# Optimization experiments

Measured on AMD Instinct MI355X. Metric: run time of the kernel, lower is better.

The kernel has to match this reference:

```python
import jax, jax.numpy as jnp
import numpy as np
from jax.ops import segment_sum, segment_max

N_NODES = 100000
N_EDGES = 1600000
F_DIM = 64
N_GRAPHS = 64
K_HOPS = 3
EPS = 1e-5


def setup_inputs() -> dict:
    key = jax.random.key(0)
    ks = jax.random.split(key, 8)
    x = jax.random.normal(ks[0], (N_NODES, F_DIM), dtype=jnp.float32)
    edge_index = jax.random.randint(ks[1], (2, N_EDGES), 0, N_NODES, dtype=jnp.int32)
    batch = jnp.sort(jax.random.randint(ks[2], (N_NODES,), 0, N_GRAPHS, dtype=jnp.int32))
    edge_weight = jax.random.uniform(ks[3], (N_EDGES,), dtype=jnp.float32)
    # TAGConv params: K+1 hop-wise linear weights (no per-lin bias) + one output bias
    W = jax.random.normal(ks[4], (K_HOPS + 1, F_DIM, F_DIM), dtype=jnp.float32) * 0.05
    b = jnp.zeros((F_DIM,), dtype=jnp.float32)
    # GraphNorm params
    gn_weight = jnp.ones((F_DIM,), dtype=jnp.float32)
    gn_bias = jnp.zeros((F_DIM,), dtype=jnp.float32)
    gn_mean_scale = jnp.ones((F_DIM,), dtype=jnp.float32)
    return {"x": x, "edge_index": edge_index, "batch": batch, "edge_weight": edge_weight,
            "W": W, "b": b, "gn_weight": gn_weight, "gn_bias": gn_bias,
            "gn_mean_scale": gn_mean_scale}


def reference(x, edge_index, batch, edge_weight, W, b, gn_weight, gn_bias, gn_mean_scale):
    src, dst = edge_index[0], edge_index[1]

    # --- TAGConv: gcn_norm without self-loops ---
    deg = segment_sum(edge_weight, dst, num_segments=N_NODES)            # [N]
    dis = jnp.where(deg > 0, jax.lax.rsqrt(deg), 0.0)                    # deg^{-1/2}, inf -> 0
    norm = dis[src] * edge_weight * dis[dst]                             # [E]

    # out = sum_k (A_norm^k x) W_k + b
    out = x @ W[0]
    h = x
    for k in range(1, K_HOPS + 1):
        h = segment_sum(norm[:, None] * h[src], dst, num_segments=N_NODES)  # [N, F]
        out = out + h @ W[k]
    out = out + b

    # --- GraphNorm: per-graph mean/var with learnable mean_scale ---
    cnt = segment_sum(jnp.ones((N_NODES,), out.dtype), batch, num_segments=N_GRAPHS)
    cnt = jnp.maximum(cnt, 1.0)[:, None]                                  # [G, 1]
    mean = segment_sum(out, batch, num_segments=N_GRAPHS) / cnt          # [G, F]
    centered = out - mean[batch] * gn_mean_scale                         # [N, F]
    var = segment_sum(centered * centered, batch, num_segments=N_GRAPHS) / cnt
    hn = gn_weight * centered / jnp.sqrt(var + EPS)[batch] + gn_bias

    # --- residual + ReLU (add_residue=True) ---
    h_emb = jax.nn.relu(hn + x)                                          # [N, F]

    # --- global mean + max pooling ---
    mean_pool = segment_sum(h_emb, batch, num_segments=N_GRAPHS) / cnt   # [G, F]
    max_pool = segment_max(h_emb, batch, num_segments=N_GRAPHS)          # [G, F]
    flat = jnp.concatenate([mean_pool, max_pool], axis=-1)               # [G, 2F]

    return (h_emb, flat)
```

## Files before the change

kernel.cpp:

```cpp
#include <hip/hip_runtime.h>
#include <hip/hip_bf16.h>

#define NN 100000
#define NE 1600000
#define NG 64
#define FD 64
#define EPSV 1e-5f

typedef __hip_bfloat16 bf16;
typedef __attribute__((ext_vector_type(8))) short bf16x8;
typedef __attribute__((ext_vector_type(4))) float f32x4;

__device__ __forceinline__ float ldb(bf16 v) { return __bfloat162float(v); }
__device__ __forceinline__ bf16 f2b(float v) { return __float2bfloat16(v); }
__device__ __forceinline__ float b2f_bits(short s) {
    return __uint_as_float(((unsigned)(unsigned short)s) << 16);
}

#define NB1 391
#define CB 625
#define EPB 2560
#define CCN (NB1 * CB)
#define SCB2 ((CCN + 2047) / 2048)

__device__ __forceinline__ int xcd_chunk(int bid, int nwg) {
    int q = nwg >> 3, r = nwg & 7;
    int xcd = bid & 7, j = bid >> 3;
    return (xcd < r ? xcd * (q + 1) : r * (q + 1) + (xcd - r) * q) + j;
}

constexpr size_t ALGN(size_t x) { return (x + 255) & ~(size_t)255; }
constexpr size_t OFF_GSUM = 0;
constexpr size_t OFF_GSSQ = OFF_GSUM + ALGN((size_t)NG * FD * 4);
constexpr size_t OFF_GCNT = OFF_GSSQ + ALGN((size_t)NG * FD * 4);
constexpr size_t OFF_PSUM = OFF_GCNT + ALGN((size_t)NG * 4);
constexpr size_t OFF_PMAX = OFF_PSUM + ALGN((size_t)NG * FD * 4);
constexpr size_t ZERO_BYTES = OFF_PMAX + ALGN((size_t)NG * FD * 4);
constexpr size_t OFF_CNT  = ZERO_BYTES;
constexpr size_t OFF_DIS  = OFF_CNT  + ALGN((size_t)NN * 4);
constexpr size_t OFF_ROWP = OFF_DIS  + ALGN((size_t)NN * 4);
constexpr size_t OFF_BSUM = OFF_ROWP + ALGN((size_t)NN * 4);
constexpr size_t OFF_WT   = OFF_BSUM + ALGN(256 * 4);
constexpr size_t OFF_CSR  = OFF_WT   + ALGN(16384 * 2);
constexpr size_t OFF_H    = OFF_CSR  + ALGN((size_t)NE * 8);
constexpr size_t OFF_OUT  = OFF_H    + ALGN((size_t)NN * 256 * 2);
constexpr size_t OFF_CSRT = OFF_OUT;
constexpr size_t OFF_CC   = OFF_CSRT + ALGN((size_t)NE * 8);
static_assert(OFF_CC + (size_t)CCN * 4 - OFF_OUT <= (size_t)NN * FD * 4, "alias overflow");

#define XCB 6250
__global__ __launch_bounds__(256) void coarse_fused_kernel(const int* __restrict__ dst,
                                                           int* __restrict__ cc,
                                                           const float* __restrict__ x,
                                                           bf16* __restrict__ H,
                                                           const float* __restrict__ W,
                                                           bf16* __restrict__ Wt) {
    int b = blockIdx.x;
    if (b < CB) {
        __shared__ int hist[NB1];
        for (int i = threadIdx.x; i < NB1; i += 256) hist[i] = 0;
        __syncthreads();
        int e0 = b * EPB + threadIdx.x;
        #pragma unroll
        for (int i = 0; i < EPB / 256; i++)
            atomicAdd(&hist[dst[e0 + i * 256] >> 8], 1);
        __syncthreads();
        for (int i = threadIdx.x; i < NB1; i += 256)
            cc[(size_t)i * CB + b] = hist[i];
    } else if (b < CB + XCB) {
        int i = (b - CB) * 256 + threadIdx.x;
        float4 xv = ((const float4*)x)[i];
        bf16 t0 = f2b(xv.x), t1 = f2b(xv.y), t2 = f2b(xv.z), t3 = f2b(xv.w);
        ushort4 o;
        o.x = *(unsigned short*)&t0; o.y = *(unsigned short*)&t1;
        o.z = *(unsigned short*)&t2; o.w = *(unsigned short*)&t3;
        ((ushort4*)H)[i] = o;
    } else {
        int i = (b - CB - XCB) * 256 + threadIdx.x;
        int n = i & 63, kk = i >> 6;
        Wt[n * 256 + kk] = f2b(W[kk * 64 + n]);
    }
}

#define SCAN_BLK 256
#define SCAN_ITEMS 8
__global__ __launch_bounds__(SCAN_BLK) void scan_blocks(int* __restrict__ data,
                                                        int* __restrict__ bsum, int n) {
    __shared__ int lds[SCAN_BLK];
    int t = threadIdx.x, b = blockIdx.x;
    int base = b * SCAN_BLK * SCAN_ITEMS + t * SCAN_ITEMS;
    int v[SCAN_ITEMS];
    int s = 0;
    #pragma unroll
    for (int i = 0; i < SCAN_ITEMS; i++) {
        int idx = base + i;
        v[i] = (idx < n) ? data[idx] : 0;
        s += v[i];
    }
    lds[t] = s;
    __syncthreads();
    for (int off = 1; off < SCAN_BLK; off <<= 1) {
        int x = (t >= off) ? lds[t - off] : 0;
        __syncthreads();
        lds[t] += x;
        __syncthreads();
    }
    int excl = lds[t] - s;
    if (t == SCAN_BLK - 1) bsum[b] = lds[t];
    int run = excl;
    #pragma unroll
    for (int i = 0; i < SCAN_ITEMS; i++) {
        int idx = base + i;
        if (idx < n) data[idx] = run;
        run += v[i];
    }
}

__global__ __launch_bounds__(256) void bsum_scan(int* __restrict__ bsum, int nb) {
    __shared__ int lds[256];
    int t = threadIdx.x;
    int v = (t < nb) ? bsum[t] : 0;
    lds[t] = v;
    __syncthreads();
    for (int off = 1; off < 256; off <<= 1) {
        int x = (t >= off) ? lds[t - off] : 0;
        __syncthreads();
        lds[t] += x;
        __syncthreads();
    }
    if (t < nb) bsum[t] = lds[t] - v;
}

__global__ __launch_bounds__(256) void scan_add2(int* __restrict__ data,
                                                 const int* __restrict__ bpref, int n) {
    int i = blockIdx.x * 256 + threadIdx.x;
    if (i >= n) return;
    data[i] += bpref[i >> 11];
}

__global__ __launch_bounds__(256) void scatter2_kernel(const int* __restrict__ src,
                                                       const int* __restrict__ dst,
                                                       const float* __restrict__ ew,
                                                       const int* __restrict__ cc,
                                                       int2* __restrict__ csrt) {
    __shared__ int sc[512];
    __shared__ int gdel[NB1];
    __shared__ int2 stage[EPB];
    __shared__ int sdel[EPB];
    int t = threadIdx.x;
    int L = xcd_chunk(blockIdx.x, CB);

    sc[t] = 0; sc[t + 256] = 0;
    __syncthreads();

    int br[EPB / 256], px[EPB / 256], pw[EPB / 256];
    #pragma unroll
    for (int i = 0; i < EPB / 256; i++) {
        int e = L * EPB + i * 256 + t;
        int d = dst[e];
        int bk = d >> 8;
        int rk = atomicAdd(&sc[bk], 1);
        br[i] = bk | (rk << 9);
        px[i] = src[e] | ((d & 255) << 17);
        pw[i] = __float_as_int(ew[e]);
    }
    __syncthreads();

    for (int off = 1; off < 512; off <<= 1) {
        int a0 = (t >= off) ? sc[t - off] : 0;
        int a1 = sc[t + 256 - off];
        __syncthreads();
        sc[t] += a0; sc[t + 256] += a1;
        __syncthreads();
    }

    for (int i = t; i < NB1; i += 256)
        gdel[i] = cc[(size_t)i * CB + L] - ((i > 0) ? sc[i - 1] : 0);
    __syncthreads();

    #pragma unroll
    for (int i = 0; i < EPB / 256; i++) {
        int bk = br[i] & 511;
        int rk = br[i] >> 9;
        int slot = ((bk > 0) ? sc[bk - 1] : 0) + rk;
        stage[slot] = make_int2(px[i], pw[i]);
        sdel[slot] = gdel[bk];
    }
    __syncthreads();

    for (int j = t; j < EPB; j += 256)
        csrt[(size_t)(sdel[j] + j)] = stage[j];
}

__global__ __launch_bounds__(256) void fine_kernel(const int* __restrict__ cc,
                                                   const int2* __restrict__ csrt,
                                                   int2* __restrict__ csr,
                                                   int* __restrict__ rowp,
                                                   int* __restrict__ cnts,
                                                   float* __restrict__ dis) {
    __shared__ int hist[256];
    __shared__ float degw[256];
    __shared__ int pref[256];
    __shared__ int fcur[256];
    int b = blockIdx.x;
    int t = threadIdx.x;
    int base = cc[(size_t)b * CB];
    int end = (b == NB1 - 1) ? NE : cc[(size_t)(b + 1) * CB];
    int cnt = end - base;
    hist[t] = 0; degw[t] = 0.f;
    __syncthreads();
    for (int j = t; j < cnt; j += 256) {
        int2 e = csrt[base + j];
        int f = e.x >> 17;
        atomicAdd(&hist[f], 1);
        atomicAdd(&degw[f], __int_as_float(e.y));
    }
    __syncthreads();
    int hv = hist[t];
    pref[t] = hv;
    __syncthreads();
    for (int off = 1; off < 256; off <<= 1) {
        int x = (t >= off) ? pref[t - off] : 0;
        __syncthreads();
        pref[t] += x;
        __syncthreads();
    }
    int ex = pref[t] - hv;
    fcur[t] = ex;
    int node = b * 256 + t;
    if (node < NN) {
        rowp[node] = base + ex;
        cnts[node] = hv;
        float s = degw[t];
        dis[node] = (s > 0.f) ? rsqrtf(s) : 0.f;
    }
    __syncthreads();
    for (int j = t; j < cnt; j += 256) {
        int2 e = csrt[base + j];
        int f = e.x >> 17;
        int pos = atomicAdd(&fcur[f], 1);
        csr[base + pos] = make_int2(e.x & 0x1FFFF, e.y);
    }
}

template <bool FIRST>
__device__ __forceinline__ void row_accum_gen(const bf16* __restrict__ hin,
                                              int2* cp, int cnt,
                                              const float* __restrict__ dis,
                                              int sub, int fl, float a[8]) {
    if (cnt <= 24) {
        int2 e0 = (sub < cnt) ? cp[sub] : make_int2(0, 0);
        int2 e1 = (8 + sub < cnt) ? cp[8 + sub] : make_int2(0, 0);
        int2 e2 = (16 + sub < cnt) ? cp[16 + sub] : make_int2(0, 0);
        bf16x8 v0 = *(const bf16x8*)(hin + (size_t)e0.x * 64 + fl * 8);
        bf16x8 v1 = *(const bf16x8*)(hin + (size_t)e1.x * 64 + fl * 8);
        bf16x8 v2 = *(const bf16x8*)(hin + (size_t)e2.x * 64 + fl * 8);
        float w0 = __int_as_float(e0.y);
        float w1 = __int_as_float(e1.y);
        float w2 = __int_as_float(e2.y);
        if (FIRST) {
            w0 *= dis[e0.x]; w1 *= dis[e1.x]; w2 *= dis[e2.x];
            if (fl == 0) {
                if (sub < cnt)      cp[sub].y      = __float_as_int(w0);
                if (8 + sub < cnt)  cp[8 + sub].y  = __float_as_int(w1);
                if (16 + sub < cnt) cp[16 + sub].y = __float_as_int(w2);
            }
        }
        #pragma unroll
        for (int i = 0; i < 8; i++)
            a[i] += w0 * b2f_bits(v0[i]) + w1 * b2f_bits(v1[i]) + w2 * b2f_bits(v2[i]);
    } else {
        float b[8] = {0, 0, 0, 0, 0, 0, 0, 0};
        int j = 0;
        for (; j + 16 <= cnt; j += 16) {
            int2 e0 = cp[j + sub];
            int2 e1 = cp[j + 8 + sub];
            bf16x8 v0 = *(const bf16x8*)(hin + (size_t)e0.x * 64 + fl * 8);
            bf16x8 v1 = *(const bf16x8*)(hin + (size_t)e1.x * 64 + fl * 8);
            float w0 = __int_as_float(e0.y);
            float w1 = __int_as_float(e1.y);
            if (FIRST) {
                w0 *= dis[e0.x]; w1 *= dis[e1.x];
                if (fl == 0) {
                    cp[j + sub].y     = __float_as_int(w0);
                    cp[j + 8 + sub].y = __float_as_int(w1);
                }
            }
            #pragma unroll
            for (int i = 0; i < 8; i++) a[i] += w0 * b2f_bits(v0[i]);
            #pragma unroll
            for (int i = 0; i < 8; i++) b[i] += w1 * b2f_bits(v1[i]);
        }
        for (; j < cnt; j += 8) {
            int jj = j + sub;
            int2 e = (jj < cnt) ? cp[jj] : make_int2(0, 0);
            bf16x8 v = *(const bf16x8*)(hin + (size_t)e.x * 64 + fl * 8);
            float w = __int_as_float(e.y);
            if (FIRST) {
                w *= dis[e.x];
                if (fl == 0 && jj < cnt) cp[jj].y = __float_as_int(w);
            }
            #pragma unroll
            for (int i = 0; i < 8; i++) a[i] += w * b2f_bits(v[i]);
        }
        #pragma unroll
        for (int i = 0; i < 8; i++) a[i] += b[i];
    }
}

template <bool FIRST>
__global__ __launch_bounds__(256) void hop_kernel(const bf16* __restrict__ hin,
                                                  bf16* __restrict__ hout,
                                                  const int* __restrict__ rowp,
                                                  const int* __restrict__ cnts,
                                                  int2* __restrict__ csr,
                                                  const float* __restrict__ dis) {
    int pair = blockIdx.x * 4 + (threadIdx.x >> 6);
    int rowA = pair * 2;
    if (rowA >= NN) return;
    rowA = __builtin_amdgcn_readfirstlane(rowA);
    int rowB = rowA + 1;
    int lane = threadIdx.x & 63;
    int sub = lane >> 3;
    int fl = lane & 7;

    int stA = rowp[rowA], cnA = cnts[rowA];
    int stB = rowp[rowB], cnB = cnts[rowB];
    float drA = dis[rowA], drB = dis[rowB];
    int2* cpA = csr + stA;
    int2* cpB = csr + stB;

    float a[8] = {0, 0, 0, 0, 0, 0, 0, 0};
    float c[8] = {0, 0, 0, 0, 0, 0, 0, 0};

    if (cnA <= 24 && cnB <= 24) {
        int2 eA0 = (sub < cnA) ? cpA[sub] : make_int2(0, 0);
        int2 eA1 = (8 + sub < cnA) ? cpA[8 + sub] : make_int2(0, 0);
        int2 eA2 = (16 + sub < cnA) ? cpA[16 + sub] : make_int2(0, 0);
        int2 eB0 = (sub < cnB) ? cpB[sub] : make_int2(0, 0);
        int2 eB1 = (8 + sub < cnB) ? cpB[8 + sub] : make_int2(0, 0);
        int2 eB2 = (16 + sub < cnB) ? cpB[16 + sub] : make_int2(0, 0);
        const bf16* hf = hin + fl * 8;
        bf16x8 vA0 = *(const bf16x8*)(hf + (size_t)eA0.x * 64);
        bf16x8 vA1 = *(const bf16x8*)(hf + (size_t)eA1.x * 64);
        bf16x8 vA2 = *(const bf16x8*)(hf + (size_t)eA2.x * 64);
        bf16x8 vB0 = *(const bf16x8*)(hf + (size_t)eB0.x * 64);
        bf16x8 vB1 = *(const bf16x8*)(hf + (size_t)eB1.x * 64);
        bf16x8 vB2 = *(const bf16x8*)(hf + (size_t)eB2.x * 64);
        float wA0 = __int_as_float(eA0.y);
        float wA1 = __int_as_float(eA1.y);
        float wA2 = __int_as_float(eA2.y);
        float wB0 = __int_as_float(eB0.y);
        float wB1 = __int_as_float(eB1.y);
        float wB2 = __int_as_float(eB2.y);
        if (FIRST) {
            wA0 *= dis[eA0.x]; wA1 *= dis[eA1.x]; wA2 *= dis[eA2.x];
            wB0 *= dis[eB0.x]; wB1 *= dis[eB1.x]; wB2 *= dis[eB2.x];
            if (fl == 0) {
                if (sub < cnA)      cpA[sub].y      = __float_as_int(wA0);
                if (8 + sub < cnA)  cpA[8 + sub].y  = __float_as_int(wA1);
                if (16 + sub < cnA) cpA[16 + sub].y = __float_as_int(wA2);
                if (sub < cnB)      cpB[sub].y      = __float_as_int(wB0);
                if (8 + sub < cnB)  cpB[8 + sub].y  = __float_as_int(wB1);
                if (16 + sub < cnB) cpB[16 + sub].y = __float_as_int(wB2);
            }
        }
        #pragma unroll
        for (int i = 0; i < 8; i++) {
            a[i] = wA0 * b2f_bits(vA0[i]) + wA1 * b2f_bits(vA1[i]) + wA2 * b2f_bits(vA2[i]);
            c[i] = wB0 * b2f_bits(vB0[i]) + wB1 * b2f_bits(vB1[i]) + wB2 * b2f_bits(vB2[i]);
        }
    } else {
        row_accum_gen<FIRST>(hin, cpA, cnA, dis, sub, fl, a);
        row_accum_gen<FIRST>(hin, cpB, cnB, dis, sub, fl, c);
    }

    #pragma unroll
    for (int i = 0; i < 8; i++) { a[i] += __shfl_xor(a[i], 8);  c[i] += __shfl_xor(c[i], 8); }
    #pragma unroll
    for (int i = 0; i < 8; i++) { a[i] += __shfl_xor(a[i], 16); c[i] += __shfl_xor(c[i], 16); }
    #pragma unroll
    for (int i = 0; i < 8; i++) { a[i] += __shfl_xor(a[i], 32); c[i] += __shfl_xor(c[i], 32); }

    if (sub == 0) {
        bf16x8 ovA, ovB;
        #pragma unroll
        for (int i = 0; i < 8; i++) {
            bf16 tA = f2b(a[i] * drA);
            bf16 tB = f2b(c[i] * drB);
            ovA[i] = *(short*)&tA;
            ovB[i] = *(short*)&tB;
        }
        *(bf16x8*)(hout + (size_t)rowA * 64 + fl * 8) = ovA;
        *(bf16x8*)(hout + (size_t)rowB * 64 + fl * 8) = ovB;
    }
}

#define GWAVES 1024
#define NT (NN / 16)

__global__ __launch_bounds__(256, 1) void gemm_kernel(const bf16* __restrict__ H,
                                                      const bf16* __restrict__ Wt,
                                                      const float* __restrict__ bias,
                                                      float* __restrict__ outb) {
    int wave = threadIdx.x >> 6;
    int lane = threadIdx.x & 63;
    int m = lane & 15, q = lane >> 4;
    int w = blockIdx.x * 4 + wave;

    bf16x8 B[4][8];
    #pragma unroll
    for (int n = 0; n < 4; n++) {
        const bf16* brow = Wt + (size_t)(n * 16 + m) * 256 + q * 8;
        #pragma unroll
        for (int ks = 0; ks < 8; ks++) B[n][ks] = *(const bf16x8*)(brow + ks * 32);
    }
    float bv[4];
    #pragma unroll
    for (int n = 0; n < 4; n++) bv[n] = bias[n * 16 + m];

    if (w >= NT) return;

    bf16x8 A0[8], A1[8];

    #define LOADA(dst_, t_)                                                      \
        {                                                                        \
            _Pragma("unroll")                                                    \
            for (int ks = 0; ks < 8; ks++)                                       \
                dst_[ks] = *(const bf16x8*)(H +                                  \
                    ((size_t)(ks >> 1) * NN + (size_t)((t_)*16 + m)) * 64 +      \
                    (ks & 1) * 32 + q * 8);                                      \
        }

    #define COMP(src_, t_)                                                   \
        {                                                                    \
            _Pragma("unroll")                                                \
            for (int n = 0; n < 4; n++) {                                    \
                f32x4 acc = {0.f, 0.f, 0.f, 0.f};                            \
                _Pragma("unroll")                                            \
                for (int ks = 0; ks < 8; ks++)                               \
                    acc = __builtin_amdgcn_mfma_f32_16x16x32_bf16(           \
                        src_[ks], B[n][ks], acc, 0, 0, 0);                   \
                _Pragma("unroll")                                            \
                for (int r = 0; r < 4; r++)                                  \
                    outb[(size_t)((t_)*16 + q * 4 + r) * 64 + n * 16 + m] =  \
                        acc[r] + bv[n];                                      \
            }                                                                \
        }

    int t = w;
    LOADA(A0, t)
    while (true) {
        int t1 = t + GWAVES;
        if (t1 < NT) LOADA(A1, t1)
        COMP(A0, t)
        if (t1 >= NT) return;
        int t2 = t1 + GWAVES;
        if (t2 < NT) LOADA(A0, t2)
        COMP(A1, t1)
        if (t2 >= NT) return;
        t = t2;
    }
    #undef LOADA
    #undef COMP
}

#define CH 32
#define STAT_WAVES ((NN + CH - 1) / CH)
#define STAT_BLOCKS ((STAT_WAVES * 64 + 255) / 256)

__global__ __launch_bounds__(256) void stats_kernel(const float* __restrict__ outb,
                                                    const int* __restrict__ batch,
                                                    float* __restrict__ gsum,
                                                    float* __restrict__ gssq,
                                                    float* __restrict__ gcnt) {
    int wid = (blockIdx.x * 256 + threadIdx.x) >> 6;
    int lane = threadIdx.x & 63;
    int n0 = wid * CH;
    if (n0 >= NN) return;
    int n1 = min(n0 + CH, NN);
    int g0 = batch[n0];
    if (n1 == n0 + CH && batch[n1 - 1] == g0) {
        float s = 0.f, s2 = 0.f;
        #pragma unroll
        for (int i = 0; i < CH; i++) {
            float v = outb[(size_t)(n0 + i) * 64 + lane];
            s += v; s2 += v * v;
        }
        atomicAdd(&gsum[g0 * 64 + lane], s);
        atomicAdd(&gssq[g0 * 64 + lane], s2);
        if (lane == 0) atomicAdd(&gcnt[g0], (float)CH);
    } else {
        int cur = g0; float s = 0.f, s2 = 0.f; int cl = 0;
        for (int i = n0; i < n1; i++) {
            int g = batch[i];
            if (g != cur) {
                atomicAdd(&gsum[cur * 64 + lane], s);
                atomicAdd(&gssq[cur * 64 + lane], s2);
                if (lane == 0) atomicAdd(&gcnt[cur], (float)cl);
                s = 0.f; s2 = 0.f; cl = 0; cur = g;
            }
            float v = outb[(size_t)i * 64 + lane];
            s += v; s2 += v * v; cl++;
        }
        atomicAdd(&gsum[cur * 64 + lane], s);
        atomicAdd(&gssq[cur * 64 + lane], s2);
        if (lane == 0) atomicAdd(&gcnt[cur], (float)cl);
    }
}

__device__ __forceinline__ void graph_mr(const float* gsum, const float* gssq,
                                         const float* gcnt, int g, int lane, float ms,
                                         float& mm, float& r) {
    float c = fmaxf(gcnt[g], 1.f);
    float mean = gsum[g * 64 + lane] / c;
    float msq = gssq[g * 64 + lane] / c;
    mm = mean * ms;
    float var = fmaxf(msq - 2.f * mm * mean + mm * mm, 0.f);
    r = rsqrtf(var + EPSV);
}

__global__ __launch_bounds__(256) void final_kernel(const float* __restrict__ outb,
                                                    const int* __restrict__ batch,
                                                    const float* __restrict__ xg,
                                                    const float* __restrict__ gsum,
                                                    const float* __restrict__ gssq,
                                                    const float* __restrict__ gcnt,
                                                    const float* __restrict__ gw_,
                                                    const float* __restrict__ gb_,
                                                    const float* __restrict__ ms_,
                                                    float* __restrict__ psum,
                                                    int* __restrict__ pmax,
                                                    float* __restrict__ hemb) {
    int wid = (blockIdx.x * 256 + threadIdx.x) >> 6;
    int lane = threadIdx.x & 63;
    int n0 = wid * CH;
    if (n0 >= NN) return;
    int n1 = min(n0 + CH, NN);
    float gw = gw_[lane], gb = gb_[lane], ms = ms_[lane];
    int g0 = batch[n0];
    if (n1 == n0 + CH && batch[n1 - 1] == g0) {
        float m, r;
        graph_mr(gsum, gssq, gcnt, g0, lane, ms, m, r);
        float ps = 0.f, pm = 0.f;
        #pragma unroll
        for (int i = 0; i < CH; i++) {
            size_t idx = (size_t)(n0 + i) * 64 + lane;
            float hn = gw * (outb[idx] - m) * r + gb;
            float he = hn + xg[idx];
            he = he > 0.f ? he : 0.f;
            hemb[idx] = he;
            ps += he;
            pm = fmaxf(pm, he);
        }
        atomicAdd(&psum[g0 * 64 + lane], ps);
        atomicMax(&pmax[g0 * 64 + lane], __float_as_int(pm));
    } else {
        int cur = g0;
        float m, r;
        graph_mr(gsum, gssq, gcnt, cur, lane, ms, m, r);
        float ps = 0.f, pm = 0.f;
        for (int i = n0; i < n1; i++) {
            int g = batch[i];
            if (g != cur) {
                atomicAdd(&psum[cur * 64 + lane], ps);
                atomicMax(&pmax[cur * 64 + lane], __float_as_int(pm));
                ps = 0.f; pm = 0.f; cur = g;
                graph_mr(gsum, gssq, gcnt, cur, lane, ms, m, r);
            }
            size_t idx = (size_t)i * 64 + lane;
            float hn = gw * (outb[idx] - m) * r + gb;
            float he = hn + xg[idx];
            he = he > 0.f ? he : 0.f;
            hemb[idx] = he;
            ps += he;
            pm = fmaxf(pm, he);
        }
        atomicAdd(&psum[cur * 64 + lane], ps);
        atomicMax(&pmax[cur * 64 + lane], __float_as_int(pm));
    }
}

__global__ __launch_bounds__(256) void pool_kernel(const float* __restrict__ psum,
                                                   const int* __restrict__ pmax,
                                                   const float* __restrict__ gcnt,
                                                   float* __restrict__ flat) {
    int i = blockIdx.x * 256 + threadIdx.x;
    if (i >= NG * FD) return;
    int g = i >> 6, f = i & 63;
    float c = fmaxf(gcnt[g], 1.f);
    flat[(size_t)g * 128 + f] = psum[i] / c;
    flat[(size_t)g * 128 + 64 + f] = __int_as_float(pmax[i]);
}

extern "C" void kernel_launch(void* const* d_in, const int* in_sizes, int n_in,
                              void* d_out, int out_size, void* d_ws, size_t ws_size,
                              hipStream_t stream) {
    const float* x = (const float*)d_in[0];
    const int* ei = (const int*)d_in[1];
    const int* batch = (const int*)d_in[2];
    const float* ew = (const float*)d_in[3];
    const float* W = (const float*)d_in[4];
    const float* bias = (const float*)d_in[5];
    const float* gnw = (const float*)d_in[6];
    const float* gnb = (const float*)d_in[7];
    const float* gms = (const float*)d_in[8];

    const int* src = ei;
    const int* dst = ei + NE;

    char* ws = (char*)d_ws;
    float* gsum = (float*)(ws + OFF_GSUM);
    float* gssq = (float*)(ws + OFF_GSSQ);
    float* gcnt = (float*)(ws + OFF_GCNT);
    float* psum = (float*)(ws + OFF_PSUM);
    int* pmax = (int*)(ws + OFF_PMAX);
    int* cnts = (int*)(ws + OFF_CNT);
    float* dis = (float*)(ws + OFF_DIS);
    int* rowp = (int*)(ws + OFF_ROWP);
    int* bsum = (int*)(ws + OFF_BSUM);
    bf16* Wt = (bf16*)(ws + OFF_WT);
    int2* csr = (int2*)(ws + OFF_CSR);
    bf16* H = (bf16*)(ws + OFF_H);
    float* outb = (float*)(ws + OFF_OUT);
    int2* csrt = (int2*)(ws + OFF_CSRT);
    int* cc = (int*)(ws + OFF_CC);

    float* hemb = (float*)d_out;
    float* flat = hemb + (size_t)NN * FD;

    hipMemsetAsync(d_ws, 0, ZERO_BYTES, stream);

    const size_t PL = (size_t)NN * 64;
    const int HOPB = (NN / 2 + 3) / 4;
    const int GFB = (NG * FD + 255) / 256;
    const int ADDB = (CCN + 255) / 256;

    coarse_fused_kernel<<<CB + XCB + 64, 256, 0, stream>>>(dst, cc, x, H, W, Wt);
    scan_blocks<<<SCB2, 256, 0, stream>>>(cc, bsum, CCN);
    bsum_scan<<<1, 256, 0, stream>>>(bsum, SCB2);
    scan_add2<<<ADDB, 256, 0, stream>>>(cc, bsum, CCN);
    scatter2_kernel<<<CB, 256, 0, stream>>>(src, dst, ew, cc, csrt);
    fine_kernel<<<NB1, 256, 0, stream>>>(cc, csrt, csr, rowp, cnts, dis);

    hop_kernel<true><<<HOPB, 256, 0, stream>>>(H, H + PL, rowp, cnts, csr, dis);
    hop_kernel<false><<<HOPB, 256, 0, stream>>>(H + PL, H + 2 * PL, rowp, cnts, csr, dis);
    hop_kernel<false><<<HOPB, 256, 0, stream>>>(H + 2 * PL, H + 3 * PL, rowp, cnts, csr, dis);

    gemm_kernel<<<GWAVES / 4, 256, 0, stream>>>(H, Wt, bias, outb);

    stats_kernel<<<STAT_BLOCKS, 256, 0, stream>>>(outb, batch, gsum, gssq, gcnt);
    final_kernel<<<STAT_BLOCKS, 256, 0, stream>>>(outb, batch, x, gsum, gssq, gcnt,
                                                  gnw, gnb, gms, psum, pmax, hemb);
    pool_kernel<<<GFB, 256, 0, stream>>>(psum, pmax, gcnt, flat);
}
```

Before: 329.3 us.

## Fold block-prefix scan into scatter/fine kernels and fuse graph stats into GEMM

Result: slower. 339.8 us (+3.2%).

```diff
diff --git a/kernel.cpp b/kernel.cpp
--- a/kernel.cpp
+++ b/kernel.cpp
@@ -116,34 +116,14 @@
     }
 }
 
-__global__ __launch_bounds__(256) void bsum_scan(int* __restrict__ bsum, int nb) {
-    __shared__ int lds[256];
-    int t = threadIdx.x;
-    int v = (t < nb) ? bsum[t] : 0;
-    lds[t] = v;
-    __syncthreads();
-    for (int off = 1; off < 256; off <<= 1) {
-        int x = (t >= off) ? lds[t - off] : 0;
-        __syncthreads();
-        lds[t] += x;
-        __syncthreads();
-    }
-    if (t < nb) bsum[t] = lds[t] - v;
-}
-
-__global__ __launch_bounds__(256) void scan_add2(int* __restrict__ data,
-                                                 const int* __restrict__ bpref, int n) {
-    int i = blockIdx.x * 256 + threadIdx.x;
-    if (i >= n) return;
-    data[i] += bpref[i >> 11];
-}
-
 __global__ __launch_bounds__(256) void scatter2_kernel(const int* __restrict__ src,
                                                        const int* __restrict__ dst,
                                                        const float* __restrict__ ew,
                                                        const int* __restrict__ cc,
+                                                       const int* __restrict__ bsum,
                                                        int2* __restrict__ csrt) {
     __shared__ int sc[512];
+    __shared__ int bp[128];
     __shared__ int gdel[NB1];
     __shared__ int2 stage[EPB];
     __shared__ int sdel[EPB];
@@ -151,6 +131,7 @@
     int L = xcd_chunk(blockIdx.x, CB);
 
     sc[t] = 0; sc[t + 256] = 0;
+    if (t < 128) bp[t] = (t < SCB2) ? bsum[t] : 0;
     __syncthreads();
 
     int br[EPB / 256], px[EPB / 256], pw[EPB / 256];
@@ -169,13 +150,19 @@
     for (int off = 1; off < 512; off <<= 1) {
         int a0 = (t >= off) ? sc[t - off] : 0;
         int a1 = sc[t + 256 - off];
+        int a2 = (off < 128 && t < 128 && t >= off) ? bp[t - off] : 0;
         __syncthreads();
         sc[t] += a0; sc[t + 256] += a1;
-        __syncthreads();
-    }
-
-    for (int i = t; i < NB1; i += 256)
-        gdel[i] = cc[(size_t)i * CB + L] - ((i > 0) ? sc[i - 1] : 0);
+        if (off < 128 && t < 128) bp[t] += a2;
+        __syncthreads();
+    }
+
+    for (int i = t; i < NB1; i += 256) {
+        int idx = i * CB + L;
+        int k = idx >> 11;
+        int gpref = (k > 0) ? bp[k - 1] : 0;
+        gdel[i] = cc[idx] + gpref - ((i > 0) ? sc[i - 1] : 0);
+    }
     __syncthreads();
 
     #pragma unroll
@@ -193,6 +180,7 @@
 }
 
 __global__ __launch_bounds__(256) void fine_kernel(const int* __restrict__ cc,
+                                                   const int* __restrict__ bsum,
                                                    const int2* __restrict__ csrt,
                                                    int2* __restrict__ csr,
                                                    int* __restrict__ rowp,
@@ -202,13 +190,32 @@
     __shared__ float degw[256];
     __shared__ int pref[256];
     __shared__ int fcur[256];
+    __shared__ int bp[128];
+    __shared__ int bounds[2];
     int b = blockIdx.x;
     int t = threadIdx.x;
-    int base = cc[(size_t)b * CB];
-    int end = (b == NB1 - 1) ? NE : cc[(size_t)(b + 1) * CB];
-    int cnt = end - base;
     hist[t] = 0; degw[t] = 0.f;
-    __syncthreads();
+    if (t < 128) bp[t] = (t < SCB2) ? bsum[t] : 0;
+    __syncthreads();
+    for (int off = 1; off < 128; off <<= 1) {
+        int x = (t < 128 && t >= off) ? bp[t - off] : 0;
+        __syncthreads();
+        if (t < 128) bp[t] += x;
+        __syncthreads();
+    }
+    if (t == 0) {
+        int i0 = b * CB, k0 = i0 >> 11;
+        bounds[0] = cc[i0] + ((k0 > 0) ? bp[k0 - 1] : 0);
+        if (b == NB1 - 1) bounds[1] = NE;
+        else {
+            int i1 = (b + 1) * CB, k1 = i1 >> 11;
+            bounds[1] = cc[i1] + ((k1 > 0) ? bp[k1 - 1] : 0);
+        }
+    }
+    __syncthreads();
+    int base = bounds[0];
+    int cnt = bounds[1] - base;
+
     for (int j = t; j < cnt; j += 256) {
         int2 e = csrt[base + j];
         int f = e.x >> 17;
@@ -402,6 +409,10 @@
 __global__ __launch_bounds__(256, 1) void gemm_kernel(const bf16* __restrict__ H,
                                                       const bf16* __restrict__ Wt,
                                                       const float* __restrict__ bias,
+                                                      const int* __restrict__ batch,
+                                                      float* __restrict__ gsum,
+                                                      float* __restrict__ gssq,
+                                                      float* __restrict__ gcnt,
                                                       float* __restrict__ outb) {
     int wave = threadIdx.x >> 6;
     int lane = threadIdx.x & 63;
@@ -432,20 +443,56 @@
                     (ks & 1) * 32 + q * 8);                                      \
         }
 
-    #define COMP(src_, t_)                                                   \
-        {                                                                    \
-            _Pragma("unroll")                                                \
-            for (int n = 0; n < 4; n++) {                                    \
-                f32x4 acc = {0.f, 0.f, 0.f, 0.f};                            \
-                _Pragma("unroll")                                            \
-                for (int ks = 0; ks < 8; ks++)                               \
-                    acc = __builtin_amdgcn_mfma_f32_16x16x32_bf16(           \
-                        src_[ks], B[n][ks], acc, 0, 0, 0);                   \
-                _Pragma("unroll")                                            \
-                for (int r = 0; r < 4; r++)                                  \
-                    outb[(size_t)((t_)*16 + q * 4 + r) * 64 + n * 16 + m] =  \
-                        acc[r] + bv[n];                                      \
-            }                                                                \
+    #define COMP(src_, t_)                                                          \
+        {                                                                           \
+            float s_[4], s2_[4], vals_[4][4];                                       \
+            _Pragma("unroll")                                                       \
+            for (int n = 0; n < 4; n++) {                                           \
+                f32x4 acc = {0.f, 0.f, 0.f, 0.f};                                   \
+                _Pragma("unroll")                                                   \
+                for (int ks = 0; ks < 8; ks++)                                      \
+                    acc = __builtin_amdgcn_mfma_f32_16x16x32_bf16(                  \
+                        src_[ks], B[n][ks], acc, 0, 0, 0);                          \
+                float ss = 0.f, ss2 = 0.f;                                          \
+                _Pragma("unroll")                                                   \
+                for (int r = 0; r < 4; r++) {                                       \
+                    float val = acc[r] + bv[n];                                     \
+                    vals_[n][r] = val;                                              \
+                    outb[(size_t)((t_)*16 + q * 4 + r) * 64 + n * 16 + m] = val;    \
+                    ss += val; ss2 += val * val;                                    \
+                }                                                                   \
+                s_[n] = ss; s2_[n] = ss2;                                           \
+            }                                                                       \
+            int gLo = batch[(t_)*16];                                               \
+            int gHi = batch[(t_)*16 + 15];                                          \
+            if (gLo == gHi) {                                                       \
+                _Pragma("unroll")                                                   \
+                for (int n = 0; n < 4; n++) {                                       \
+                    s_[n] += __shfl_xor(s_[n], 16);  s_[n] += __shfl_xor(s_[n], 32);   \
+                    s2_[n] += __shfl_xor(s2_[n], 16); s2_[n] += __shfl_xor(s2_[n], 32);\
+                }                                                                   \
+                if (q == 0) {                                                       \
+                    _Pragma("unroll")                                               \
+                    for (int n = 0; n < 4; n++) {                                   \
+                        atomicAdd(&gsum[gLo * 64 + n * 16 + m], s_[n]);             \
+                        atomicAdd(&gssq[gLo * 64 + n * 16 + m], s2_[n]);            \
+                    }                                                               \
+                }                                                                   \
+                if (lane == 0) atomicAdd(&gcnt[gLo], 16.f);                         \
+            } else {                                                               \
+                int4 b4 = *(const int4*)(batch + (t_)*16 + q * 4);                  \
+                int gr_[4] = {b4.x, b4.y, b4.z, b4.w};                              \
+                _Pragma("unroll")                                                   \
+                for (int r = 0; r < 4; r++) {                                       \
+                    _Pragma("unroll")                                               \
+                    for (int n = 0; n < 4; n++) {                                   \
+                        atomicAdd(&gsum[gr_[r] * 64 + n * 16 + m], vals_[n][r]);    \
+                        atomicAdd(&gssq[gr_[r] * 64 + n * 16 + m],                  \
+                                  vals_[n][r] * vals_[n][r]);                       \
+                    }                                                               \
+                }                                                                   \
+                if (lane < 16) atomicAdd(&gcnt[batch[(t_)*16 + lane]], 1.f);        \
+            }                                                                       \
         }
 
     int t = w;
@@ -468,46 +515,6 @@
 #define CH 32
 #define STAT_WAVES ((NN + CH - 1) / CH)
 #define STAT_BLOCKS ((STAT_WAVES * 64 + 255) / 256)
-
-__global__ __launch_bounds__(256) void stats_kernel(const float* __restrict__ outb,
-                                                    const int* __restrict__ batch,
-                                                    float* __restrict__ gsum,
-                                                    float* __restrict__ gssq,
-                                                    float* __restrict__ gcnt) {
-    int wid = (blockIdx.x * 256 + threadIdx.x) >> 6;
-    int lane = threadIdx.x & 63;
-    int n0 = wid * CH;
-    if (n0 >= NN) return;
-    int n1 = min(n0 + CH, NN);
-    int g0 = batch[n0];
-    if (n1 == n0 + CH && batch[n1 - 1] == g0) {
-        float s = 0.f, s2 = 0.f;
-        #pragma unroll
-        for (int i = 0; i < CH; i++) {
-            float v = outb[(size_t)(n0 + i) * 64 + lane];
-            s += v; s2 += v * v;
-        }
-        atomicAdd(&gsum[g0 * 64 + lane], s);
-        atomicAdd(&gssq[g0 * 64 + lane], s2);
-        if (lane == 0) atomicAdd(&gcnt[g0], (float)CH);
-    } else {
-        int cur = g0; float s = 0.f, s2 = 0.f; int cl = 0;
-        for (int i = n0; i < n1; i++) {
-            int g = batch[i];
-            if (g != cur) {
-                atomicAdd(&gsum[cur * 64 + lane], s);
-                atomicAdd(&gssq[cur * 64 + lane], s2);
-                if (lane == 0) atomicAdd(&gcnt[cur], (float)cl);
-                s = 0.f; s2 = 0.f; cl = 0; cur = g;
-            }
-            float v = outb[(size_t)i * 64 + lane];
-            s += v; s2 += v * v; cl++;
-        }
-        atomicAdd(&gsum[cur * 64 + lane], s);
-        atomicAdd(&gssq[cur * 64 + lane], s2);
-        if (lane == 0) atomicAdd(&gcnt[cur], (float)cl);
-    }
-}
 
 __device__ __forceinline__ void graph_mr(const float* gsum, const float* gssq,
                                          const float* gcnt, int g, int lane, float ms,
@@ -634,22 +641,18 @@
     const size_t PL = (size_t)NN * 64;
     const int HOPB = (NN / 2 + 3) / 4;
     const int GFB = (NG * FD + 255) / 256;
-    const int ADDB = (CCN + 255) / 256;
 
     coarse_fused_kernel<<<CB + XCB + 64, 256, 0, stream>>>(dst, cc, x, H, W, Wt);
     scan_blocks<<<SCB2, 256, 0, stream>>>(cc, bsum, CCN);
-    bsum_scan<<<1, 256, 0, stream>>>(bsum, SCB2);
-    scan_add2<<<ADDB, 256, 0, stream>>>(cc, bsum, CCN);
-    scatter2_kernel<<<CB, 256, 0, stream>>>(src, dst, ew, cc, csrt);
-    fine_kernel<<<NB1, 256, 0, stream>>>(cc, csrt, csr, rowp, cnts, dis);
+    scatter2_kernel<<<CB, 256, 0, stream>>>(src, dst, ew, cc, bsum, csrt);
+    fine_kernel<<<NB1, 256, 0, stream>>>(cc, bsum, csrt, csr, rowp, cnts, dis);
 
     hop_kernel<true><<<HOPB, 256, 0, stream>>>(H, H + PL, rowp, cnts, csr, dis);
     hop_kernel<false><<<HOPB, 256, 0, stream>>>(H + PL, H + 2 * PL, rowp, cnts, csr, dis);
     hop_kernel<false><<<HOPB, 256, 0, stream>>>(H + 2 * PL, H + 3 * PL, rowp, cnts, csr, dis);
 
-    gemm_kernel<<<GWAVES / 4, 256, 0, stream>>>(H, Wt, bias, outb);
-
-    stats_kernel<<<STAT_BLOCKS, 256, 0, stream>>>(outb, batch, gsum, gssq, gcnt);
+    gemm_kernel<<<GWAVES / 4, 256, 0, stream>>>(H, Wt, bias, batch, gsum, gssq, gcnt, outb);
+
     final_kernel<<<STAT_BLOCKS, 256, 0, stream>>>(outb, batch, x, gsum, gssq, gcnt,
                                                   gnw, gnb, gms, psum, pmax, hemb);
     pool_kernel<<<GFB, 256, 0, stream>>>(psum, pmax, gcnt, flat);
```
